# Kernel tuning notes

Measured on AMD Instinct MI355X. Metric: run time of the kernel, lower is better.

Reference implementation:

```python
import jax, jax.numpy as jnp
from jax import lax
import numpy as np

B, N, H = 8, 2048, 128
THRESH = 0.3


def setup_inputs() -> dict:
    key = jax.random.key(0)
    k1, k2, k3 = jax.random.split(key, 3)
    node_embeddings = jax.random.normal(k1, (B * N, H), jnp.float32)
    # contiguous equal-sized graphs, as produced by PyG-style batching
    batch = jnp.repeat(jnp.arange(B, dtype=jnp.int64), N)
    # path_scorer params: Linear(2H->H) then Linear(H->1)
    W1 = jax.random.normal(k2, (2 * H, H), jnp.float32) * 0.02  # input-major
    b1 = jnp.zeros((H,), jnp.float32)
    W2 = jax.random.normal(k3, (H,), jnp.float32) * 0.02
    b2 = jnp.zeros((), jnp.float32)
    return {"node_embeddings": node_embeddings, "batch": batch,
            "W1": W1, "b1": b1, "W2": W2, "b2": b2}


def _run(emb, W1, b1, W2, b2):
    """emb: [B, N, H]. Returns (path [B,N] int32 padded with -1, scores [B,N])."""
    Bn, Nn, Hh = emb.shape
    bidx = jnp.arange(Bn)
    nidx = jnp.arange(Nn)
    # split first Linear: score(i,j) = sigmoid(w2 . elu(e_i@W1a + e_j@W1b + b1) + b2)
    A = jnp.einsum('bnh,hk->bnk', emb, W1[:Hh])          # current-node half [B,N,H]
    C = jnp.einsum('bnh,hk->bnk', emb, W1[Hh:]) + b1     # neighbor half + bias [B,N,H]
    root = jnp.argmax(emb[:, :, 0], axis=1)              # [B]
    visited0 = jnp.zeros((Bn, Nn), bool).at[bidx, root].set(True)

    def step(carry, _):
        cur, visited, active = carry
        # score every node against the current node in one fused pass
        h = jax.nn.elu(A[bidx, cur][:, None, :] + C)                      # [B,N,H]
        s = jax.nn.sigmoid(jnp.einsum('bnh,h->bn', h, W2) + b2)           # [B,N]
        sm = jnp.where(visited, -jnp.inf, s)
        best = jnp.argmax(sm, axis=1)                                     # first max == stable sort
        bscore = jnp.take_along_axis(sm, best[:, None], axis=1)[:, 0]
        take = active & (bscore > THRESH)
        visited = visited | (take[:, None] & (nidx[None, :] == best[:, None]))
        new_cur = jnp.where(take, best, cur)
        step_path = jnp.where(take, best, -1).astype(jnp.int32)
        step_score = jnp.where(take, bscore, 0.0).astype(emb.dtype)
        return (new_cur, visited, take), (step_path, step_score)

    init = (root, visited0, jnp.ones((Bn,), bool))
    _, (paths, scoreseq) = lax.scan(step, init, None, length=Nn - 1)
    path = jnp.concatenate([root[:, None].astype(jnp.int32), paths.T], axis=1)      # [B,N]
    scores = jnp.concatenate([jnp.ones((Bn, 1), emb.dtype), scoreseq.T], axis=1)    # root score = 1.0
    return path, scores


def reference(node_embeddings, batch, W1, b1, W2, b2):
    num_graphs = int(batch[-1]) + 1  # contiguous equal-sized graphs
    emb = node_embeddings.reshape(num_graphs, -1, node_embeddings.shape[-1])
    return _run(emb, W1, b1, W2, b2)
```

## Files before the change

kernel.cpp:

```cpp
#include <hip/hip_runtime.h>
#include <math.h>

#define B_ 8
#define N_ 2048
#define H_ 128
#define BN_ (B_ * N_)


__device__ __forceinline__ float elu1(float x) {
    return x > 0.f ? x : (__expf(x) - 1.f);
}

__device__ __forceinline__ unsigned enc_key(float v) {
    unsigned u = __float_as_uint(v);
    return (u & 0x80000000u) ? ~u : (u | 0x80000000u);
}
__device__ __forceinline__ float dec_key(unsigned k) {
    return __uint_as_float((k & 0x80000000u) ? (k & 0x7FFFFFFFu) : ~k);
}

__global__ __launch_bounds__(H_) void k_ac(const float* __restrict__ emb,
                                           const float* __restrict__ W1,
                                           const float* __restrict__ b1,
                                           float* __restrict__ A,
                                           float* __restrict__ C) {
    __shared__ float e[H_];
    const int i = blockIdx.x;
    const int k = threadIdx.x;
    e[k] = emb[(size_t)i * H_ + k];
    __syncthreads();
    float a = 0.f, c = 0.f;
#pragma unroll 8
    for (int h = 0; h < H_; ++h) {
        const float ev = e[h];
        a = fmaf(ev, W1[h * H_ + k], a);
        c = fmaf(ev, W1[(H_ + h) * H_ + k], c);
    }
    A[(size_t)i * H_ + k] = a;
    C[(size_t)i * H_ + k] = c + b1[k];
}

__global__ __launch_bounds__(256) void k_z(const float* __restrict__ A,
                                           const float* __restrict__ Cc,
                                           const float* __restrict__ w2,
                                           const float* __restrict__ b2p,
                                           unsigned* __restrict__ K) {
    const int lane = threadIdx.x & 63;
    const int wave = threadIdx.x >> 6;
    const int g = blockIdx.x >> 8;
    const int sub = blockIdx.x & 255;
    const int rowtile = sub & 127;
    const int jh = sub >> 7;
    const int ibase = rowtile * 16 + wave * 4;
    const int i = ibase + (lane & 3);
    const int he = (lane >> 2) * 8;
    const float b2v = *b2p;

    const float* Arow = A + ((size_t)g * N_ + i) * H_ + he;
    const float4 a0 = *(const float4*)(Arow);
    const float4 a1 = *(const float4*)(Arow + 4);
    const float4 w0 = *(const float4*)(w2 + he);
    const float4 w1v = *(const float4*)(w2 + he + 4);
    const float* Cg = Cc + (size_t)g * N_ * H_ + he;
    unsigned* Krow = K + ((size_t)g * N_ + i) * N_;
    const bool writer = ((lane >> 2) == 0);

    const int j0 = jh * 1024;
    for (int j = j0; j < j0 + 1024; j += 8) {
        float4 c0[8], c1[8];
#pragma unroll
        for (int q = 0; q < 8; ++q) {
            const float* Cj = Cg + (size_t)(j + q) * H_;
            c0[q] = *(const float4*)(Cj);
            c1[q] = *(const float4*)(Cj + 4);
        }
        float pv[8];
#pragma unroll
        for (int q = 0; q < 8; ++q) {
            float p = 0.f;
            p = fmaf(w0.x, elu1(a0.x + c0[q].x), p);
            p = fmaf(w0.y, elu1(a0.y + c0[q].y), p);
            p = fmaf(w0.z, elu1(a0.z + c0[q].z), p);
            p = fmaf(w0.w, elu1(a0.w + c0[q].w), p);
            p = fmaf(w1v.x, elu1(a1.x + c1[q].x), p);
            p = fmaf(w1v.y, elu1(a1.y + c1[q].y), p);
            p = fmaf(w1v.z, elu1(a1.z + c1[q].z), p);
            p = fmaf(w1v.w, elu1(a1.w + c1[q].w), p);
            pv[q] = p;
        }
#pragma unroll
        for (int q = 0; q < 8; ++q) pv[q] += __shfl_xor(pv[q], 4);
#pragma unroll
        for (int q = 0; q < 8; ++q) pv[q] += __shfl_xor(pv[q], 8);
#pragma unroll
        for (int q = 0; q < 8; ++q) pv[q] += __shfl_xor(pv[q], 16);
#pragma unroll
        for (int q = 0; q < 8; ++q) pv[q] += __shfl_xor(pv[q], 32);
        if (writer) {
            uint4 ka, kb;
            ka.x = enc_key(pv[0] + b2v);
            ka.y = enc_key(pv[1] + b2v);
            ka.z = enc_key(pv[2] + b2v);
            ka.w = enc_key(pv[3] + b2v);
            kb.x = enc_key(pv[4] + b2v);
            kb.y = enc_key(pv[5] + b2v);
            kb.z = enc_key(pv[6] + b2v);
            kb.w = enc_key(pv[7] + b2v);
            *(uint4*)(Krow + j) = ka;
            *(uint4*)(Krow + j + 4) = kb;
        }
    }
}

__global__ __launch_bounds__(64, 1) void k_path4(const float* __restrict__ emb,
                                                 const unsigned* __restrict__ K,
                                                 float* __restrict__ out) {
    const int g = blockIdx.x;
    const int lane = threadIdx.x;

    unsigned lo[32];
#pragma unroll
    for (int k = 0; k < 8; ++k)
#pragma unroll
        for (int e = 0; e < 4; ++e)
            lo[k * 4 + e] = ~(unsigned)(k * 256 + (lane << 2) + e);

    float bv0 = -INFINITY;
    int bi0 = 0x7fffffff;
    for (int j = lane; j < N_; j += 64) {
        const float v = emb[((size_t)g * N_ + j) * H_];
        if (v > bv0) { bv0 = v; bi0 = j; }
    }
#pragma unroll
    for (int off = 1; off < 64; off <<= 1) {
        const float ov = __shfl_xor(bv0, off);
        const int oi = __shfl_xor(bi0, off);
        if (ov > bv0 || (ov == bv0 && oi < bi0)) { bv0 = ov; bi0 = oi; }
    }
    int cur = bi0;
    unsigned vbits = 0;
    if (((cur >> 2) & 63) == lane)
        vbits |= 1u << (((cur >> 8) << 2) | (cur & 3));

    float* pathOut = out + (size_t)g * N_;
    float* scoreOut = out + (size_t)BN_ + (size_t)g * N_;
    if (lane == 0) {
        pathOut[0] = (float)cur;
        scoreOut[0] = 1.0f;
    }

    const unsigned* Kg = K + (size_t)g * N_ * N_;
    uint4 z[8], z2[8];
    {
        const uint4* Kr = (const uint4*)(Kg + ((size_t)cur << 11));
#pragma unroll
        for (int k = 0; k < 8; ++k) z[k] = Kr[k * 64 + lane];
    }
    int pred = -1;

    int t = 1;
    for (; t < N_; ++t) {
        unsigned long long kk[32];
#pragma unroll
        for (int k = 0; k < 8; ++k) {
            const unsigned zx = z[k].x, zy = z[k].y, zz = z[k].z, zw = z[k].w;
            const int b = k * 4;
            kk[b + 0] = ((unsigned long long)(((vbits >> (b + 0)) & 1u) ? 0u : zx) << 32) | lo[b + 0];
            kk[b + 1] = ((unsigned long long)(((vbits >> (b + 1)) & 1u) ? 0u : zy) << 32) | lo[b + 1];
            kk[b + 2] = ((unsigned long long)(((vbits >> (b + 2)) & 1u) ? 0u : zz) << 32) | lo[b + 2];
            kk[b + 3] = ((unsigned long long)(((vbits >> (b + 3)) & 1u) ? 0u : zw) << 32) | lo[b + 3];
        }
#pragma unroll
        for (int s = 16; s >= 1; s >>= 1)
#pragma unroll
            for (int i = 0; i < s; ++i)
                if (kk[i + s] > kk[i]) kk[i] = kk[i + s];
        const unsigned long long lanebest = kk[0];
        unsigned long long key = lanebest;
#pragma unroll
        for (int off = 1; off < 64; off <<= 1) {
            const unsigned long long ok = __shfl_xor(key, off);
            if (ok > key) key = ok;
        }
        const int bi = (int)(~(unsigned)key);

        if (bi == pred) {
#pragma unroll
            for (int k = 0; k < 8; ++k) z[k] = z2[k];
        } else {
            const uint4* Kr = (const uint4*)(Kg + ((size_t)bi << 11));
#pragma unroll
            for (int k = 0; k < 8; ++k) z[k] = Kr[k * 64 + lane];
        }

        unsigned long long pk = (lanebest == key) ? 0ull : lanebest;
#pragma unroll
        for (int off = 1; off < 64; off <<= 1) {
            const unsigned long long ok = __shfl_xor(pk, off);
            if (ok > pk) pk = ok;
        }
        int np = (pk == 0ull) ? -1 : (int)(~(unsigned)pk);
        {
            const int safe = (np >= 0) ? np : bi;
            const uint4* Kr2 = (const uint4*)(Kg + ((size_t)safe << 11));
#pragma unroll
            for (int k = 0; k < 8; ++k) z2[k] = Kr2[k * 64 + lane];
        }
        pred = np;

        const float bv = dec_key((unsigned)(key >> 32));
        const float s = 1.f / (1.f + expf(-bv));
        if (!((double)s > 0.3)) break;
        cur = bi;
        if (((cur >> 2) & 63) == lane)
            vbits |= 1u << (((cur >> 8) << 2) | (cur & 3));
        if (lane == 0) {
            pathOut[t] = (float)cur;
            scoreOut[t] = s;
        }
    }
    for (int tt = t + lane; tt < N_; tt += 64) {
        pathOut[tt] = -1.f;
        scoreOut[tt] = 0.f;
    }
}

__device__ __forceinline__ void blockArgmax(float& bv, int& bi, float* rv, int* ri,
                                            int lane, int wid, int nw) {
#pragma unroll
    for (int off = 1; off < 64; off <<= 1) {
        const float ov = __shfl_xor(bv, off);
        const int oi = __shfl_xor(bi, off);
        if (ov > bv || (ov == bv && oi < bi)) { bv = ov; bi = oi; }
    }
    if (lane == 0) { rv[wid] = bv; ri[wid] = bi; }
    __syncthreads();
    if (wid == 0) {
        float v = (lane < nw) ? rv[lane] : -INFINITY;
        int ix = (lane < nw) ? ri[lane] : 0x7fffffff;
#pragma unroll
        for (int off = 1; off < 16; off <<= 1) {
            const float ov = __shfl_xor(v, off);
            const int oi = __shfl_xor(ix, off);
            if (ov > v || (ov == v && oi < ix)) { v = ov; ix = oi; }
        }
        if (lane == 0) { rv[0] = v; ri[0] = ix; }
    }
    __syncthreads();
    bv = rv[0];
    bi = ri[0];
}

__global__ __launch_bounds__(1024) void k_path_fly(const float* __restrict__ emb,
                                                   const float* __restrict__ A,
                                                   const float* __restrict__ Cc,
                                                   const float* __restrict__ w2g,
                                                   const float* __restrict__ b2p,
                                                   float* __restrict__ out) {
    const int g = blockIdx.x;
    const int tid = threadIdx.x;
    const int lane = tid & 63, wid = tid >> 6;
    __shared__ float acur[H_], w2s[H_];
    __shared__ unsigned char vis[N_];
    __shared__ float rv[16];
    __shared__ int ri[16];
    const float b2v = *b2p;
    if (tid < H_) w2s[tid] = w2g[tid];
    for (int j = tid; j < N_; j += 1024) vis[j] = 0;

    float bv = -INFINITY;
    int bi = 0x7fffffff;
    for (int j = tid; j < N_; j += 1024) {
        const float v = emb[((size_t)g * N_ + j) * H_];
        if (v > bv) { bv = v; bi = j; }
    }
    __syncthreads();
    blockArgmax(bv, bi, rv, ri, lane, wid, 16);
    int cur = bi;
    float* pathOut = out + (size_t)g * N_;
    float* scoreOut = out + (size_t)BN_ + (size_t)g * N_;
    if (tid == 0) {
        vis[cur] = 1;
        pathOut[0] = (float)cur;
        scoreOut[0] = 1.0f;
    }
    __syncthreads();

    int t = 1;
    for (; t < N_; ++t) {
        if (tid < H_) acur[tid] = A[((size_t)g * N_ + cur) * H_ + tid];
        __syncthreads();
        float mbv = -INFINITY;
        int mbi = 0x7fffffff;
#pragma unroll
        for (int q = 0; q < 2; ++q) {
            const int j = tid + q * 1024;
            const float* Cj = Cc + ((size_t)g * N_ + j) * H_;
            float p = 0.f;
            for (int h = 0; h < H_; h += 4) {
                const float4 c = *(const float4*)(Cj + h);
                p = fmaf(w2s[h + 0], elu1(acur[h + 0] + c.x), p);
                p = fmaf(w2s[h + 1], elu1(acur[h + 1] + c.y), p);
                p = fmaf(w2s[h + 2], elu1(acur[h + 2] + c.z), p);
                p = fmaf(w2s[h + 3], elu1(acur[h + 3] + c.w), p);
            }
            const float z = p + b2v;
            if (!vis[j] && (z > mbv || (z == mbv && j < mbi))) { mbv = z; mbi = j; }
        }
        __syncthreads();
        blockArgmax(mbv, mbi, rv, ri, lane, wid, 16);
        const float s = 1.f / (1.f + expf(-mbv));
        if (!((double)s > 0.3)) break;
        cur = mbi;
        if (tid == 0) {
            vis[cur] = 1;
            pathOut[t] = (float)cur;
            scoreOut[t] = s;
        }
        __syncthreads();
    }
    for (int tt = t + tid; tt < N_; tt += 1024) {
        pathOut[tt] = -1.f;
        scoreOut[tt] = 0.f;
    }
}

extern "C" void kernel_launch(void* const* d_in, const int* in_sizes, int n_in,
                              void* d_out, int out_size, void* d_ws, size_t ws_size,
                              hipStream_t stream) {
    (void)in_sizes; (void)n_in; (void)out_size;
    const float* emb = (const float*)d_in[0];
    const float* W1 = (const float*)d_in[2];
    const float* b1 = (const float*)d_in[3];
    const float* w2 = (const float*)d_in[4];
    const float* b2 = (const float*)d_in[5];
    float* out = (float*)d_out;

    float* A = (float*)d_ws;
    float* C = A + (size_t)BN_ * H_;
    unsigned* K = (unsigned*)(C + (size_t)BN_ * H_);
    const size_t need = ((size_t)BN_ * H_ * 2 + (size_t)B_ * N_ * N_) * sizeof(float);

    hipLaunchKernelGGL(k_ac, dim3(BN_), dim3(H_), 0, stream, emb, W1, b1, A, C);
    if (ws_size >= need) {
        hipLaunchKernelGGL(k_z, dim3(2048), dim3(256), 0, stream, A, C, w2, b2, K);
        hipLaunchKernelGGL(k_path4, dim3(B_), dim3(64), 0, stream, emb, K, out);
    } else {
        hipLaunchKernelGGL(k_path_fly, dim3(B_), dim3(1024), 0, stream,
                           emb, A, C, w2, b2, out);
    }
}
```

Before: 3.730 ms.

## Use 32-bit argmax with ballot tie-break and drop speculative second-best row prefetch

```diff
diff --git a/kernel.cpp b/kernel.cpp
--- a/kernel.cpp
+++ b/kernel.cpp
@@ -112,18 +112,11 @@
     }
 }
 
-__global__ __launch_bounds__(64, 1) void k_path4(const float* __restrict__ emb,
+__global__ __launch_bounds__(64, 1) void k_path5(const float* __restrict__ emb,
                                                  const unsigned* __restrict__ K,
                                                  float* __restrict__ out) {
     const int g = blockIdx.x;
     const int lane = threadIdx.x;
-
-    unsigned lo[32];
-#pragma unroll
-    for (int k = 0; k < 8; ++k)
-#pragma unroll
-        for (int e = 0; e < 4; ++e)
-            lo[k * 4 + e] = ~(unsigned)(k * 256 + (lane << 2) + e);
 
     float bv0 = -INFINITY;
     int bi0 = 0x7fffffff;
@@ -150,65 +143,63 @@
     }
 
     const unsigned* Kg = K + (size_t)g * N_ * N_;
-    uint4 z[8], z2[8];
+    uint4 z[8];
     {
         const uint4* Kr = (const uint4*)(Kg + ((size_t)cur << 11));
 #pragma unroll
         for (int k = 0; k < 8; ++k) z[k] = Kr[k * 64 + lane];
     }
-    int pred = -1;
 
     int t = 1;
     for (; t < N_; ++t) {
-        unsigned long long kk[32];
-#pragma unroll
-        for (int k = 0; k < 8; ++k) {
-            const unsigned zx = z[k].x, zy = z[k].y, zz = z[k].z, zw = z[k].w;
-            const int b = k * 4;
-            kk[b + 0] = ((unsigned long long)(((vbits >> (b + 0)) & 1u) ? 0u : zx) << 32) | lo[b + 0];
-            kk[b + 1] = ((unsigned long long)(((vbits >> (b + 1)) & 1u) ? 0u : zy) << 32) | lo[b + 1];
-            kk[b + 2] = ((unsigned long long)(((vbits >> (b + 2)) & 1u) ? 0u : zz) << 32) | lo[b + 2];
-            kk[b + 3] = ((unsigned long long)(((vbits >> (b + 3)) & 1u) ? 0u : zw) << 32) | lo[b + 3];
-        }
-#pragma unroll
-        for (int s = 16; s >= 1; s >>= 1)
-#pragma unroll
-            for (int i = 0; i < s; ++i)
-                if (kk[i + s] > kk[i]) kk[i] = kk[i + s];
-        const unsigned long long lanebest = kk[0];
-        unsigned long long key = lanebest;
+        unsigned best = 0u;
+        int bj = 0;
+#define SLOT(KRAW, S)                                                   \
+        {                                                               \
+            const unsigned kv_ = ((vbits >> (S)) & 1u) ? 0u : (KRAW);   \
+            if (kv_ >= best) { best = kv_; bj = (S); }                  \
+        }
+        SLOT(z[7].w, 31) SLOT(z[7].z, 30) SLOT(z[7].y, 29) SLOT(z[7].x, 28)
+        SLOT(z[6].w, 27) SLOT(z[6].z, 26) SLOT(z[6].y, 25) SLOT(z[6].x, 24)
+        SLOT(z[5].w, 23) SLOT(z[5].z, 22) SLOT(z[5].y, 21) SLOT(z[5].x, 20)
+        SLOT(z[4].w, 19) SLOT(z[4].z, 18) SLOT(z[4].y, 17) SLOT(z[4].x, 16)
+        SLOT(z[3].w, 15) SLOT(z[3].z, 14) SLOT(z[3].y, 13) SLOT(z[3].x, 12)
+        SLOT(z[2].w, 11) SLOT(z[2].z, 10) SLOT(z[2].y,  9) SLOT(z[2].x,  8)
+        SLOT(z[1].w,  7) SLOT(z[1].z,  6) SLOT(z[1].y,  5) SLOT(z[1].x,  4)
+        SLOT(z[0].w,  3) SLOT(z[0].z,  2) SLOT(z[0].y,  1) SLOT(z[0].x,  0)
+#undef SLOT
+
+        unsigned w = best;
 #pragma unroll
         for (int off = 1; off < 64; off <<= 1) {
-            const unsigned long long ok = __shfl_xor(key, off);
-            if (ok > key) key = ok;
-        }
-        const int bi = (int)(~(unsigned)key);
-
-        if (bi == pred) {
-#pragma unroll
-            for (int k = 0; k < 8; ++k) z[k] = z2[k];
+            const unsigned ow = __shfl_xor(w, off);
+            if (ow > w) w = ow;
+        }
+        const unsigned long long mk = __ballot(best == w);
+        int bi;
+        if (__popcll(mk) == 1) {
+            const int src = (int)(__ffsll((long long)mk) - 1);
+            const int bjw = __shfl(bj, src);
+            bi = ((bjw >> 2) << 8) | (src << 2) | (bjw & 3);
         } else {
+            unsigned cand = (best == w)
+                ? ~(unsigned)(((bj >> 2) << 8) | (lane << 2) | (bj & 3))
+                : 0u;
+#pragma unroll
+            for (int off = 1; off < 64; off <<= 1) {
+                const unsigned oc = __shfl_xor(cand, off);
+                if (oc > cand) cand = oc;
+            }
+            bi = (int)(~cand);
+        }
+
+        {
             const uint4* Kr = (const uint4*)(Kg + ((size_t)bi << 11));
 #pragma unroll
             for (int k = 0; k < 8; ++k) z[k] = Kr[k * 64 + lane];
         }
 
-        unsigned long long pk = (lanebest == key) ? 0ull : lanebest;
-#pragma unroll
-        for (int off = 1; off < 64; off <<= 1) {
-            const unsigned long long ok = __shfl_xor(pk, off);
-            if (ok > pk) pk = ok;
-        }
-        int np = (pk == 0ull) ? -1 : (int)(~(unsigned)pk);
-        {
-            const int safe = (np >= 0) ? np : bi;
-            const uint4* Kr2 = (const uint4*)(Kg + ((size_t)safe << 11));
-#pragma unroll
-            for (int k = 0; k < 8; ++k) z2[k] = Kr2[k * 64 + lane];
-        }
-        pred = np;
-
-        const float bv = dec_key((unsigned)(key >> 32));
+        const float bv = dec_key(w);
         const float s = 1.f / (1.f + expf(-bv));
         if (!((double)s > 0.3)) break;
         cur = bi;
@@ -344,7 +335,7 @@
     hipLaunchKernelGGL(k_ac, dim3(BN_), dim3(H_), 0, stream, emb, W1, b1, A, C);
     if (ws_size >= need) {
         hipLaunchKernelGGL(k_z, dim3(2048), dim3(256), 0, stream, A, C, w2, b2, K);
-        hipLaunchKernelGGL(k_path4, dim3(B_), dim3(64), 0, stream, emb, K, out);
+        hipLaunchKernelGGL(k_path5, dim3(B_), dim3(64), 0, stream, emb, K, out);
     } else {
         hipLaunchKernelGGL(k_path_fly, dim3(B_), dim3(1024), 0, stream,
                            emb, A, C, w2, b2, out);
```

Measured after the change: 3.218 ms. -13.7%, faster.
